# Kernel tuning notes

Measured on AMD Instinct MI355X. Metric: run time of the kernel, lower is better.

The kernel has to match this reference:

```python
import jax, jax.numpy as jnp
import numpy as np

B, T, C, H = 2, 2048, 1024, 16
HD = C // H  # head dim = 64


def setup_inputs() -> dict:
    key = jax.random.key(0)
    k1, k2, k3 = jax.random.split(key, 3)
    x = jax.random.normal(k1, (B, T, C), dtype=jnp.float32)
    W_attn = jax.random.normal(k2, (C, 3 * C), dtype=jnp.float32) * (C ** -0.5)
    W_proj = jax.random.normal(k3, (C, C), dtype=jnp.float32) * (C ** -0.5)
    b_proj = jnp.zeros((C,), dtype=jnp.float32)
    return {"x": x, "W_attn": W_attn, "W_proj": W_proj, "b_proj": b_proj}


def reference(x, W_attn, W_proj, b_proj):
    Bv, Tv, Cv = x.shape
    qkv = x @ W_attn  # [B, T, 3C]  (no bias: config.bias=False)
    # NOTE: source splits as k, q, v (k first!)
    k, q, v = jnp.split(qkv, 3, axis=2)
    # [B, H, T, HD]
    q = q.reshape(Bv, Tv, H, HD).transpose(0, 2, 1, 3)
    k = k.reshape(Bv, Tv, H, HD).transpose(0, 2, 1, 3)
    v = v.reshape(Bv, Tv, H, HD).transpose(0, 2, 1, 3)
    wei = jnp.einsum('bhqd,bhkd->bhqk', q, k) * (HD ** -0.5)
    causal = jnp.tril(jnp.ones((Tv, Tv), dtype=bool))
    wei = jnp.where(causal, wei, -jnp.inf)
    wei = jax.nn.softmax(wei, axis=-1)
    # dropout = 0.0 (eval) -> identity
    out = jnp.einsum('bhqk,bhkd->bhqd', wei, v)
    out = out.transpose(0, 2, 1, 3).reshape(Bv, Tv, Cv)
    out = out @ W_proj + b_proj
    return out
```

## Files before the change

kernel.cpp:

```cpp
#include <hip/hip_runtime.h>

typedef __attribute__((ext_vector_type(8))) short short8;
typedef __attribute__((ext_vector_type(4))) short short4v;
typedef __attribute__((ext_vector_type(4))) float float4v;

#define T_SEQ 2048
#define CDIM 1024
#define NHEAD 16
#define HDIM 64
#define LROW 40
#define PROW 72

__device__ __forceinline__ unsigned short f2bf(float f) {
    unsigned u = __builtin_bit_cast(unsigned, f);
    u += 0x7FFF + ((u >> 16) & 1);
    return (unsigned short)(u >> 16);
}

__global__ __launch_bounds__(256) void convert_f32_bf16_vec(
    const float* __restrict__ in, unsigned short* __restrict__ out) {
    int i = blockIdx.x * 256 + threadIdx.x;
    float4 v = ((const float4*)in)[i];
    ushort4 o;
    o.x = f2bf(v.x); o.y = f2bf(v.y); o.z = f2bf(v.z); o.w = f2bf(v.w);
    ((ushort4*)out)[i] = o;
}

__global__ __launch_bounds__(256) void transpose_f32_bf16(
    const float* __restrict__ in, unsigned short* __restrict__ out, int K, int N) {
    __shared__ float tile[32][33];
    int kb = blockIdx.x * 32, nb = blockIdx.y * 32;
    int tx = threadIdx.x & 31, ty = threadIdx.x >> 5;
    for (int r = 0; r < 4; r++)
        tile[ty + r * 8][tx] = in[(size_t)(kb + ty + r * 8) * N + nb + tx];
    __syncthreads();
    for (int r = 0; r < 4; r++)
        out[(size_t)(nb + ty + r * 8) * K + kb + tx] = f2bf(tile[tx][ty + r * 8]);
}

__global__ __launch_bounds__(256) void gemm_qkv(
    const unsigned short* __restrict__ A, const unsigned short* __restrict__ Bt,
    unsigned short* __restrict__ dK, unsigned short* __restrict__ dQ,
    unsigned short* __restrict__ dV) {
    const int K = 1024;
    const int NITER = K / 32;
    __shared__ unsigned short sA[2][128 * LROW];
    __shared__ unsigned short sB[2][128 * LROW];
    int tid = threadIdx.x, wave = tid >> 6, lane = tid & 63;
    int quad = lane >> 4, l16 = lane & 15;
    int wm = wave >> 1, wn = wave & 1;
    int blockM = blockIdx.y * 128, blockN = blockIdx.x * 128;
    int rlane = lane >> 2, seg = lane & 3;
    bool swapAB = (blockN >= 2048);

    const unsigned short* gA = A + (size_t)blockM * K;
    const unsigned short* gB = Bt + (size_t)blockN * K;

    float4v acc[4][4] = {};
    uint4 ra[2], rb[2];

    int srow[2], soff[2];
    for (int i = 0; i < 2; i++) {
        srow[i] = wave * 32 + i * 16 + rlane;
        soff[i] = srow[i] * LROW + seg * 8;
    }

    for (int i = 0; i < 2; i++) {
        ra[i] = *(const uint4*)(gA + (size_t)srow[i] * K + seg * 8);
        rb[i] = *(const uint4*)(gB + (size_t)srow[i] * K + seg * 8);
    }
    for (int i = 0; i < 2; i++) {
        *(uint4*)(sA[0] + soff[i]) = ra[i];
        *(uint4*)(sB[0] + soff[i]) = rb[i];
    }

    int aoff = (wm * 64 + l16) * LROW + quad * 8;
    int boff = (wn * 64 + l16) * LROW + quad * 8;

    for (int it = 0; it < NITER; it++) {
        int cur = it & 1;
        __syncthreads();
        if (it + 1 < NITER) {
            int kb = (it + 1) * 32;
            for (int i = 0; i < 2; i++) {
                ra[i] = *(const uint4*)(gA + (size_t)srow[i] * K + kb + seg * 8);
                rb[i] = *(const uint4*)(gB + (size_t)srow[i] * K + kb + seg * 8);
            }
        }
        const unsigned short* cA = sA[cur];
        const unsigned short* cB = sB[cur];
        short8 af[4], bf[4];
        for (int i = 0; i < 4; i++)
            af[i] = *(const short8*)(cA + aoff + i * 16 * LROW);
        for (int j = 0; j < 4; j++)
            bf[j] = *(const short8*)(cB + boff + j * 16 * LROW);
        if (!swapAB) {
            for (int i = 0; i < 4; i++)
                for (int j = 0; j < 4; j++)
                    acc[i][j] = __builtin_amdgcn_mfma_f32_16x16x32_bf16(
                        af[i], bf[j], acc[i][j], 0, 0, 0);
        } else {
            for (int i = 0; i < 4; i++)
                for (int j = 0; j < 4; j++)
                    acc[i][j] = __builtin_amdgcn_mfma_f32_16x16x32_bf16(
                        bf[j], af[i], acc[i][j], 0, 0, 0);
        }
        if (it + 1 < NITER) {
            int nxt = cur ^ 1;
            for (int i = 0; i < 2; i++) {
                *(uint4*)(sA[nxt] + soff[i]) = ra[i];
                *(uint4*)(sB[nxt] + soff[i]) = rb[i];
            }
        }
    }

    if (!swapAB) {
        const float QSCL = 0.18033688011112042f;
        for (int i = 0; i < 4; i++)
            for (int j = 0; j < 4; j++)
                for (int r = 0; r < 4; r++) {
                    int m = blockM + wm * 64 + i * 16 + quad * 4 + r;
                    int n = blockN + wn * 64 + j * 16 + l16;
                    int part = n >> 10, c = n & 1023;
                    int h = c >> 6, d = c & 63;
                    int bb = m >> 11, t = m & 2047;
                    int bh = bb * NHEAD + h;
                    if (part == 0) {
                        dK[(((size_t)bh * T_SEQ + t) << 6) + d] = f2bf(acc[i][j][r]);
                    } else {
                        dQ[(((size_t)bh * T_SEQ + t) << 6) + d] =
                            f2bf(acc[i][j][r] * QSCL);
                    }
                }
    } else {
        for (int i = 0; i < 4; i++)
            for (int j = 0; j < 4; j++)
                for (int r = 0; r < 4; r++) {
                    int n = blockN + wn * 64 + j * 16 + quad * 4 + r;
                    int m = blockM + wm * 64 + i * 16 + l16;
                    int c = n & 1023;
                    int h = c >> 6, d = c & 63;
                    int bb = m >> 11, t = m & 2047;
                    int bh = bb * NHEAD + h;
                    dV[((size_t)bh * HDIM + d) * T_SEQ + t] = f2bf(acc[i][j][r]);
                }
    }
}

__global__ __launch_bounds__(256) void gemm_proj(
    const unsigned short* __restrict__ A, const unsigned short* __restrict__ Bt,
    const float* __restrict__ bias, float* __restrict__ out) {
    const int K = 1024;
    const int NITER = K / 64;
    __shared__ unsigned short sA[2][64 * PROW];
    __shared__ unsigned short sB[2][64 * PROW];
    int tid = threadIdx.x, wave = tid >> 6, lane = tid & 63;
    int quad = lane >> 4, l16 = lane & 15;
    int wm = wave >> 1, wn = wave & 1;
    int blockM = blockIdx.y * 64, blockN = blockIdx.x * 64;

    int srow = tid >> 3;
    int sseg = tid & 7;
    const unsigned short* gA0 = A + (size_t)(blockM + srow) * K + sseg * 8;
    const unsigned short* gA1 = gA0 + (size_t)32 * K;
    const unsigned short* gB0 = Bt + (size_t)(blockN + srow) * K + sseg * 8;
    const unsigned short* gB1 = gB0 + (size_t)32 * K;
    int so0 = srow * PROW + sseg * 8;
    int so1 = (srow + 32) * PROW + sseg * 8;

    float4v acc[2][2] = {};
    uint4 ra0, ra1, rb0, rb1;

    ra0 = *(const uint4*)gA0; ra1 = *(const uint4*)gA1;
    rb0 = *(const uint4*)gB0; rb1 = *(const uint4*)gB1;
    *(uint4*)(sA[0] + so0) = ra0;
    *(uint4*)(sA[0] + so1) = ra1;
    *(uint4*)(sB[0] + so0) = rb0;
    *(uint4*)(sB[0] + so1) = rb1;

    int aoff = (wm * 32 + l16) * PROW + quad * 8;
    int boff = (wn * 32 + l16) * PROW + quad * 8;

    for (int it = 0; it < NITER; it++) {
        int cur = it & 1;
        __syncthreads();
        if (it + 1 < NITER) {
            int kb = (it + 1) * 64;
            ra0 = *(const uint4*)(gA0 + kb); ra1 = *(const uint4*)(gA1 + kb);
            rb0 = *(const uint4*)(gB0 + kb); rb1 = *(const uint4*)(gB1 + kb);
        }
        const unsigned short* cA = sA[cur];
        const unsigned short* cB = sB[cur];
        short8 af[2][2], bf[2][2];
        for (int i = 0; i < 2; i++)
            for (int k = 0; k < 2; k++)
                af[i][k] = *(const short8*)(cA + aoff + i * 16 * PROW + k * 32);
        for (int j = 0; j < 2; j++)
            for (int k = 0; k < 2; k++)
                bf[j][k] = *(const short8*)(cB + boff + j * 16 * PROW + k * 32);
        for (int i = 0; i < 2; i++)
            for (int j = 0; j < 2; j++) {
                acc[i][j] = __builtin_amdgcn_mfma_f32_16x16x32_bf16(
                    af[i][0], bf[j][0], acc[i][j], 0, 0, 0);
                acc[i][j] = __builtin_amdgcn_mfma_f32_16x16x32_bf16(
                    af[i][1], bf[j][1], acc[i][j], 0, 0, 0);
            }
        if (it + 1 < NITER) {
            int nxt = cur ^ 1;
            *(uint4*)(sA[nxt] + so0) = ra0;
            *(uint4*)(sA[nxt] + so1) = ra1;
            *(uint4*)(sB[nxt] + so0) = rb0;
            *(uint4*)(sB[nxt] + so1) = rb1;
        }
    }

    for (int i = 0; i < 2; i++)
        for (int j = 0; j < 2; j++)
            for (int r = 0; r < 4; r++) {
                int m = blockM + wm * 32 + i * 16 + quad * 4 + r;
                int n = blockN + wn * 32 + j * 16 + l16;
                out[(size_t)m * CDIM + n] = acc[i][j][r] + bias[n];
            }
}

__global__ __launch_bounds__(256) void attn_fwd(
    const unsigned short* __restrict__ Qp, const unsigned short* __restrict__ Kp,
    const unsigned short* __restrict__ Vt, unsigned short* __restrict__ att) {
    __shared__ unsigned short sK[2][64 * 72];
    __shared__ unsigned short sV[2][64 * 72];
    int tid = threadIdx.x, wave = tid >> 6, lane = tid & 63;
    int quad = lane >> 4, l16 = lane & 15;
    int bh = blockIdx.x;
    int bb = bh >> 4, h = bh & 15;
    size_t baseQ = (size_t)bh * T_SEQ * HDIM;
    size_t baseV = (size_t)bh * HDIM * T_SEQ;
    int row4 = tid >> 2, seg = tid & 3;

    int xt = 31 - blockIdx.y;
    int qb = xt * 64;
    int qrow = qb + wave * 16 + l16;

    const unsigned short* qr = Qp + baseQ + (size_t)qrow * HDIM;
    short8 qf0 = *(const short8*)(qr + quad * 8);
    short8 qf1 = *(const short8*)(qr + 32 + quad * 8);

    float4v o[4] = {};
    float lsum = 0.f;
    int nt = xt + 1;

    uint4 ka, kb2, va, vb;
    {
        const unsigned short* gk = Kp + baseQ + (size_t)row4 * HDIM + seg * 16;
        const unsigned short* gv = Vt + baseV + (size_t)row4 * T_SEQ + seg * 16;
        ka = *(const uint4*)gk; kb2 = *(const uint4*)(gk + 8);
        va = *(const uint4*)gv; vb = *(const uint4*)(gv + 8);
    }
    *(uint4*)(sK[0] + row4 * 72 + seg * 16) = ka;
    *(uint4*)(sK[0] + row4 * 72 + seg * 16 + 8) = kb2;
    *(uint4*)(sV[0] + row4 * 72 + seg * 16) = va;
    *(uint4*)(sV[0] + row4 * 72 + seg * 16 + 8) = vb;

    for (int t = 0; t < nt; t++) {
        int cur = t & 1;
        __syncthreads();
        if (t + 1 < nt) {
            const unsigned short* gk =
                Kp + baseQ + (size_t)((t + 1) * 64 + row4) * HDIM + seg * 16;
            const unsigned short* gv =
                Vt + baseV + (size_t)row4 * T_SEQ + (t + 1) * 64 + seg * 16;
            ka = *(const uint4*)gk; kb2 = *(const uint4*)(gk + 8);
            va = *(const uint4*)gv; vb = *(const uint4*)(gv + 8);
        }

        const unsigned short* cK = sK[cur];
        const unsigned short* cV = sV[cur];
        float4v s[4];
        for (int sub = 0; sub < 4; sub++) {
            short8 kf0 = *(const short8*)(cK + (sub * 16 + l16) * 72 + quad * 8);
            short8 kf1 =
                *(const short8*)(cK + (sub * 16 + l16) * 72 + 32 + quad * 8);
            float4v z = {};
            z = __builtin_amdgcn_mfma_f32_16x16x32_bf16(kf0, qf0, z, 0, 0, 0);
            z = __builtin_amdgcn_mfma_f32_16x16x32_bf16(kf1, qf1, z, 0, 0, 0);
            s[sub] = z;
        }

        bool need_mask = (t * 64 + 63) > (qb + wave * 16);
        float p[16];
        for (int sub = 0; sub < 4; sub++)
            for (int r = 0; r < 4; r++) {
                float v = s[sub][r];
                if (need_mask) {
                    int kg = t * 64 + sub * 16 + quad * 4 + r;
                    v = (kg <= qrow) ? v : -1e30f;
                }
                p[sub * 4 + r] = v;
            }
        unsigned ub[16];
        for (int i = 0; i < 16; i++) {
            float e = exp2f(p[i] - 16.0f);
            unsigned u = __builtin_bit_cast(unsigned, e) & 0xffff0000u;
            ub[i] = u;
            lsum += __builtin_bit_cast(float, u);
        }

        for (int sub = 0; sub < 4; sub++) {
            unsigned lo = __builtin_amdgcn_perm(ub[sub * 4 + 1], ub[sub * 4 + 0],
                                                0x07060302u);
            unsigned hi = __builtin_amdgcn_perm(ub[sub * 4 + 3], ub[sub * 4 + 2],
                                                0x07060302u);
            uint2 packed = {lo, hi};
            short4v pf = __builtin_bit_cast(short4v, packed);
            for (int dc = 0; dc < 4; dc++) {
                short4v vf = *(const short4v*)(
                    cV + (dc * 16 + l16) * 72 + sub * 16 + quad * 4);
                o[dc] = __builtin_amdgcn_mfma_f32_16x16x16bf16_1k(
                    vf, pf, o[dc], 0, 0, 0);
            }
        }

        if (t + 1 < nt) {
            int nxt = cur ^ 1;
            *(uint4*)(sK[nxt] + row4 * 72 + seg * 16) = ka;
            *(uint4*)(sK[nxt] + row4 * 72 + seg * 16 + 8) = kb2;
            *(uint4*)(sV[nxt] + row4 * 72 + seg * 16) = va;
            *(uint4*)(sV[nxt] + row4 * 72 + seg * 16 + 8) = vb;
        }
    }

    lsum += __shfl_xor(lsum, 16);
    lsum += __shfl_xor(lsum, 32);
    float inv = 1.0f / lsum;

    __syncthreads();
    for (int dc = 0; dc < 4; dc++) {
        short4v ov;
        for (int r = 0; r < 4; r++) ov[r] = (short)f2bf(o[dc][r] * inv);
        *(short4v*)(sK[0] + wave * 1152 + l16 * 72 + dc * 16 + quad * 4) = ov;
    }
    __syncthreads();
    int orow = lane >> 2, oseg = lane & 3;
    uint4 a = *(const uint4*)(sK[0] + wave * 1152 + orow * 72 + oseg * 16);
    uint4 b = *(const uint4*)(sK[0] + wave * 1152 + orow * 72 + oseg * 16 + 8);
    unsigned short* dst = att +
        (size_t)(bb * T_SEQ + qb + wave * 16 + orow) * CDIM + h * HDIM +
        oseg * 16;
    *(uint4*)dst = a;
    *(uint4*)(dst + 8) = b;
}

extern "C" void kernel_launch(void* const* d_in, const int* in_sizes, int n_in,
                              void* d_out, int out_size, void* d_ws, size_t ws_size,
                              hipStream_t stream) {
    const float* x      = (const float*)d_in[0];
    const float* W_attn = (const float*)d_in[1];
    const float* W_proj = (const float*)d_in[2];
    const float* b_proj = (const float*)d_in[3];
    float* out = (float*)d_out;

    unsigned short* xb   = (unsigned short*)d_ws;
    unsigned short* WaT  = xb  + 4096 * 1024;
    unsigned short* WpT  = WaT + 3072 * 1024;
    unsigned short* Karr = WpT + 1024 * 1024;
    unsigned short* Qarr = Karr + 2 * 16 * 2048 * 64;
    unsigned short* Varr = Qarr + 2 * 16 * 2048 * 64;
    unsigned short* attb = Varr + 2 * 16 * 2048 * 64;

    convert_f32_bf16_vec<<<4096, 256, 0, stream>>>(x, xb);
    transpose_f32_bf16<<<dim3(32, 96), 256, 0, stream>>>(W_attn, WaT, 1024, 3072);
    transpose_f32_bf16<<<dim3(32, 32), 256, 0, stream>>>(W_proj, WpT, 1024, 1024);
    gemm_qkv<<<dim3(24, 32), 256, 0, stream>>>(xb, WaT, Karr, Qarr, Varr);
    attn_fwd<<<dim3(32, 32), 256, 0, stream>>>(Qarr, Karr, Varr, attb);
    gemm_proj<<<dim3(16, 64), 256, 0, stream>>>(attb, WpT, b_proj, out);
}
```

Baseline: 199.8 us.

## Enlarge proj GEMM tiles and read K/V directly from global in attention

The output projection GEMM moves from 64x64 tiles with a K-step of 64 to 128x128 tiles with a K-step of 32, giving each wave a 4x4 MFMA accumulator block, and the bias loads are hoisted. The attention kernel drops its shared-memory double buffering of K and V. Each wave now loads K/V fragments straight from global memory (relying on L1/L2 caching), which removes the per-tile __syncthreads barriers. s_setprio hints are added around the MFMA sections. The proj GEMM now launches only 256 blocks, which may underfill the GPU, and the direct global loads in attention risk added memory latency and redundant traffic across the four waves.

```diff
diff --git a/kernel.cpp b/kernel.cpp
--- a/kernel.cpp
+++ b/kernel.cpp
@@ -9,7 +9,6 @@
 #define NHEAD 16
 #define HDIM 64
 #define LROW 40
-#define PROW 72
 
 __device__ __forceinline__ unsigned short f2bf(float f) {
     unsigned u = __builtin_bit_cast(unsigned, f);
@@ -151,90 +150,90 @@
     const unsigned short* __restrict__ A, const unsigned short* __restrict__ Bt,
     const float* __restrict__ bias, float* __restrict__ out) {
     const int K = 1024;
-    const int NITER = K / 64;
-    __shared__ unsigned short sA[2][64 * PROW];
-    __shared__ unsigned short sB[2][64 * PROW];
+    const int NITER = K / 32;
+    __shared__ unsigned short sA[2][128 * LROW];
+    __shared__ unsigned short sB[2][128 * LROW];
     int tid = threadIdx.x, wave = tid >> 6, lane = tid & 63;
     int quad = lane >> 4, l16 = lane & 15;
     int wm = wave >> 1, wn = wave & 1;
-    int blockM = blockIdx.y * 64, blockN = blockIdx.x * 64;
-
-    int srow = tid >> 3;
-    int sseg = tid & 7;
-    const unsigned short* gA0 = A + (size_t)(blockM + srow) * K + sseg * 8;
-    const unsigned short* gA1 = gA0 + (size_t)32 * K;
-    const unsigned short* gB0 = Bt + (size_t)(blockN + srow) * K + sseg * 8;
-    const unsigned short* gB1 = gB0 + (size_t)32 * K;
-    int so0 = srow * PROW + sseg * 8;
-    int so1 = (srow + 32) * PROW + sseg * 8;
-
-    float4v acc[2][2] = {};
-    uint4 ra0, ra1, rb0, rb1;
-
-    ra0 = *(const uint4*)gA0; ra1 = *(const uint4*)gA1;
-    rb0 = *(const uint4*)gB0; rb1 = *(const uint4*)gB1;
-    *(uint4*)(sA[0] + so0) = ra0;
-    *(uint4*)(sA[0] + so1) = ra1;
-    *(uint4*)(sB[0] + so0) = rb0;
-    *(uint4*)(sB[0] + so1) = rb1;
-
-    int aoff = (wm * 32 + l16) * PROW + quad * 8;
-    int boff = (wn * 32 + l16) * PROW + quad * 8;
+    int blockM = blockIdx.y * 128, blockN = blockIdx.x * 128;
+    int rlane = lane >> 2, seg = lane & 3;
+
+    const unsigned short* gA = A + (size_t)blockM * K;
+    const unsigned short* gB = Bt + (size_t)blockN * K;
+
+    float4v acc[4][4] = {};
+    uint4 ra[2], rb[2];
+
+    int srow[2], soff[2];
+    for (int i = 0; i < 2; i++) {
+        srow[i] = wave * 32 + i * 16 + rlane;
+        soff[i] = srow[i] * LROW + seg * 8;
+    }
+
+    for (int i = 0; i < 2; i++) {
+        ra[i] = *(const uint4*)(gA + (size_t)srow[i] * K + seg * 8);
+        rb[i] = *(const uint4*)(gB + (size_t)srow[i] * K + seg * 8);
+    }
+    for (int i = 0; i < 2; i++) {
+        *(uint4*)(sA[0] + soff[i]) = ra[i];
+        *(uint4*)(sB[0] + soff[i]) = rb[i];
+    }
+
+    int aoff = (wm * 64 + l16) * LROW + quad * 8;
+    int boff = (wn * 64 + l16) * LROW + quad * 8;
 
     for (int it = 0; it < NITER; it++) {
         int cur = it & 1;
         __syncthreads();
         if (it + 1 < NITER) {
-            int kb = (it + 1) * 64;
-            ra0 = *(const uint4*)(gA0 + kb); ra1 = *(const uint4*)(gA1 + kb);
-            rb0 = *(const uint4*)(gB0 + kb); rb1 = *(const uint4*)(gB1 + kb);
+            int kb = (it + 1) * 32;
+            for (int i = 0; i < 2; i++) {
+                ra[i] = *(const uint4*)(gA + (size_t)srow[i] * K + kb + seg * 8);
+                rb[i] = *(const uint4*)(gB + (size_t)srow[i] * K + kb + seg * 8);
+            }
         }
         const unsigned short* cA = sA[cur];
         const unsigned short* cB = sB[cur];
-        short8 af[2][2], bf[2][2];
-        for (int i = 0; i < 2; i++)
-            for (int k = 0; k < 2; k++)
-                af[i][k] = *(const short8*)(cA + aoff + i * 16 * PROW + k * 32);
-        for (int j = 0; j < 2; j++)
-            for (int k = 0; k < 2; k++)
-                bf[j][k] = *(const short8*)(cB + boff + j * 16 * PROW + k * 32);
-        for (int i = 0; i < 2; i++)
-            for (int j = 0; j < 2; j++) {
+        short8 af[4], bf[4];
+        for (int i = 0; i < 4; i++)
+            af[i] = *(const short8*)(cA + aoff + i * 16 * LROW);
+        for (int j = 0; j < 4; j++)
+            bf[j] = *(const short8*)(cB + boff + j * 16 * LROW);
+        for (int i = 0; i < 4; i++)
+            for (int j = 0; j < 4; j++)
                 acc[i][j] = __builtin_amdgcn_mfma_f32_16x16x32_bf16(
-                    af[i][0], bf[j][0], acc[i][j], 0, 0, 0);
-                acc[i][j] = __builtin_amdgcn_mfma_f32_16x16x32_bf16(
-                    af[i][1], bf[j][1], acc[i][j], 0, 0, 0);
-            }
+                    af[i], bf[j], acc[i][j], 0, 0, 0);
         if (it + 1 < NITER) {
             int nxt = cur ^ 1;
-            *(uint4*)(sA[nxt] + so0) = ra0;
-            *(uint4*)(sA[nxt] + so1) = ra1;
-            *(uint4*)(sB[nxt] + so0) = rb0;
-            *(uint4*)(sB[nxt] + so1) = rb1;
-        }
-    }
-
-    for (int i = 0; i < 2; i++)
-        for (int j = 0; j < 2; j++)
+            for (int i = 0; i < 2; i++) {
+                *(uint4*)(sA[nxt] + soff[i]) = ra[i];
+                *(uint4*)(sB[nxt] + soff[i]) = rb[i];
+            }
+        }
+    }
+
+    float bv[4];
+    for (int j = 0; j < 4; j++) bv[j] = bias[blockN + wn * 64 + j * 16 + l16];
+    for (int i = 0; i < 4; i++)
+        for (int j = 0; j < 4; j++)
             for (int r = 0; r < 4; r++) {
-                int m = blockM + wm * 32 + i * 16 + quad * 4 + r;
-                int n = blockN + wn * 32 + j * 16 + l16;
-                out[(size_t)m * CDIM + n] = acc[i][j][r] + bias[n];
+                int m = blockM + wm * 64 + i * 16 + quad * 4 + r;
+                int n = blockN + wn * 64 + j * 16 + l16;
+                out[(size_t)m * CDIM + n] = acc[i][j][r] + bv[j];
             }
 }
 
 __global__ __launch_bounds__(256) void attn_fwd(
     const unsigned short* __restrict__ Qp, const unsigned short* __restrict__ Kp,
     const unsigned short* __restrict__ Vt, unsigned short* __restrict__ att) {
-    __shared__ unsigned short sK[2][64 * 72];
-    __shared__ unsigned short sV[2][64 * 72];
+    __shared__ unsigned short so[4 * 16 * 72];
     int tid = threadIdx.x, wave = tid >> 6, lane = tid & 63;
     int quad = lane >> 4, l16 = lane & 15;
     int bh = blockIdx.x;
     int bb = bh >> 4, h = bh & 15;
     size_t baseQ = (size_t)bh * T_SEQ * HDIM;
     size_t baseV = (size_t)bh * HDIM * T_SEQ;
-    int row4 = tid >> 2, seg = tid & 3;
 
     int xt = 31 - blockIdx.y;
     int qb = xt * 64;
@@ -244,46 +243,28 @@
     short8 qf0 = *(const short8*)(qr + quad * 8);
     short8 qf1 = *(const short8*)(qr + 32 + quad * 8);
 
+    const unsigned short* Kb = Kp + baseQ;
+    const unsigned short* Vb = Vt + baseV;
+
     float4v o[4] = {};
     float lsum = 0.f;
     int nt = xt + 1;
 
-    uint4 ka, kb2, va, vb;
-    {
-        const unsigned short* gk = Kp + baseQ + (size_t)row4 * HDIM + seg * 16;
-        const unsigned short* gv = Vt + baseV + (size_t)row4 * T_SEQ + seg * 16;
-        ka = *(const uint4*)gk; kb2 = *(const uint4*)(gk + 8);
-        va = *(const uint4*)gv; vb = *(const uint4*)(gv + 8);
-    }
-    *(uint4*)(sK[0] + row4 * 72 + seg * 16) = ka;
-    *(uint4*)(sK[0] + row4 * 72 + seg * 16 + 8) = kb2;
-    *(uint4*)(sV[0] + row4 * 72 + seg * 16) = va;
-    *(uint4*)(sV[0] + row4 * 72 + seg * 16 + 8) = vb;
-
     for (int t = 0; t < nt; t++) {
-        int cur = t & 1;
-        __syncthreads();
-        if (t + 1 < nt) {
-            const unsigned short* gk =
-                Kp + baseQ + (size_t)((t + 1) * 64 + row4) * HDIM + seg * 16;
-            const unsigned short* gv =
-                Vt + baseV + (size_t)row4 * T_SEQ + (t + 1) * 64 + seg * 16;
-            ka = *(const uint4*)gk; kb2 = *(const uint4*)(gk + 8);
-            va = *(const uint4*)gv; vb = *(const uint4*)(gv + 8);
-        }
-
-        const unsigned short* cK = sK[cur];
-        const unsigned short* cV = sV[cur];
+        const unsigned short* kt = Kb + (size_t)(t * 64) * HDIM;
         float4v s[4];
+        __builtin_amdgcn_s_setprio(1);
         for (int sub = 0; sub < 4; sub++) {
-            short8 kf0 = *(const short8*)(cK + (sub * 16 + l16) * 72 + quad * 8);
+            short8 kf0 =
+                *(const short8*)(kt + (sub * 16 + l16) * HDIM + quad * 8);
             short8 kf1 =
-                *(const short8*)(cK + (sub * 16 + l16) * 72 + 32 + quad * 8);
+                *(const short8*)(kt + (sub * 16 + l16) * HDIM + 32 + quad * 8);
             float4v z = {};
             z = __builtin_amdgcn_mfma_f32_16x16x32_bf16(kf0, qf0, z, 0, 0, 0);
             z = __builtin_amdgcn_mfma_f32_16x16x32_bf16(kf1, qf1, z, 0, 0, 0);
             s[sub] = z;
         }
+        __builtin_amdgcn_s_setprio(0);
 
         bool need_mask = (t * 64 + 63) > (qb + wave * 16);
         float p[16];
@@ -304,6 +285,7 @@
             lsum += __builtin_bit_cast(float, u);
         }
 
+        __builtin_amdgcn_s_setprio(1);
         for (int sub = 0; sub < 4; sub++) {
             unsigned lo = __builtin_amdgcn_perm(ub[sub * 4 + 1], ub[sub * 4 + 0],
                                                 0x07060302u);
@@ -313,35 +295,28 @@
             short4v pf = __builtin_bit_cast(short4v, packed);
             for (int dc = 0; dc < 4; dc++) {
                 short4v vf = *(const short4v*)(
-                    cV + (dc * 16 + l16) * 72 + sub * 16 + quad * 4);
+                    Vb + (size_t)(dc * 16 + l16) * T_SEQ + t * 64 + sub * 16 +
+                    quad * 4);
                 o[dc] = __builtin_amdgcn_mfma_f32_16x16x16bf16_1k(
                     vf, pf, o[dc], 0, 0, 0);
             }
         }
-
-        if (t + 1 < nt) {
-            int nxt = cur ^ 1;
-            *(uint4*)(sK[nxt] + row4 * 72 + seg * 16) = ka;
-            *(uint4*)(sK[nxt] + row4 * 72 + seg * 16 + 8) = kb2;
-            *(uint4*)(sV[nxt] + row4 * 72 + seg * 16) = va;
-            *(uint4*)(sV[nxt] + row4 * 72 + seg * 16 + 8) = vb;
-        }
+        __builtin_amdgcn_s_setprio(0);
     }
 
     lsum += __shfl_xor(lsum, 16);
     lsum += __shfl_xor(lsum, 32);
     float inv = 1.0f / lsum;
 
-    __syncthreads();
     for (int dc = 0; dc < 4; dc++) {
         short4v ov;
         for (int r = 0; r < 4; r++) ov[r] = (short)f2bf(o[dc][r] * inv);
-        *(short4v*)(sK[0] + wave * 1152 + l16 * 72 + dc * 16 + quad * 4) = ov;
+        *(short4v*)(so + wave * 1152 + l16 * 72 + dc * 16 + quad * 4) = ov;
     }
     __syncthreads();
     int orow = lane >> 2, oseg = lane & 3;
-    uint4 a = *(const uint4*)(sK[0] + wave * 1152 + orow * 72 + oseg * 16);
-    uint4 b = *(const uint4*)(sK[0] + wave * 1152 + orow * 72 + oseg * 16 + 8);
+    uint4 a = *(const uint4*)(so + wave * 1152 + orow * 72 + oseg * 16);
+    uint4 b = *(const uint4*)(so + wave * 1152 + orow * 72 + oseg * 16 + 8);
     unsigned short* dst = att +
         (size_t)(bb * T_SEQ + qb + wave * 16 + orow) * CDIM + h * HDIM +
         oseg * 16;
@@ -371,5 +346,5 @@
     transpose_f32_bf16<<<dim3(32, 32), 256, 0, stream>>>(W_proj, WpT, 1024, 1024);
     gemm_qkv<<<dim3(24, 32), 256, 0, stream>>>(xb, WaT, Karr, Qarr, Varr);
     attn_fwd<<<dim3(32, 32), 256, 0, stream>>>(Qarr, Karr, Varr, attb);
-    gemm_proj<<<dim3(16, 64), 256, 0, stream>>>(attb, WpT, b_proj, out);
-}
+    gemm_proj<<<dim3(8, 32), 256, 0, stream>>>(attb, WpT, b_proj, out);
+}
```

Measured after the change: 366.6 us. 1.83x slower.
